# Optimization experiments

Measured on AMD Instinct MI355X. Metric: run time of the kernel, lower is better.

The kernel has to match this reference:

```python
import jax, jax.numpy as jnp
import numpy as np

B, C, H, W = 4, 256, 64, 64
N = H * W


def _c1(Wt, x, b=None):
    # 1x1 conv2d: Wt [out,in], x [B,in,H,W]
    r = jnp.einsum('oi,bihw->bohw', Wt, x)
    return r if b is None else r + b[None, :, None, None]


def setup_inputs() -> dict:
    key = jax.random.key(0)
    ks = jax.random.split(key, 32)
    s = 0.01  # torch init: normal(0, 0.01)
    d = {
        'x': jax.random.normal(ks[0], (B, C, H, W), jnp.float32),
        'y': jax.random.normal(ks[1], (B, C, H, W), jnp.float32),
        'z': jax.random.normal(ks[2], (B, C, 6, 6), jnp.float32),
        'm': jax.random.normal(ks[3], (B, C, 3, 3), jnp.float32),
        'Wv':  jax.random.normal(ks[4], (C, C), jnp.float32) * s,   # conv_value, no bias
        'Wv2': jax.random.normal(ks[5], (C, C), jnp.float32) * s,   # conv_value_2, no bias
        'Wq':  jax.random.normal(ks[6], (C, C), jnp.float32) * s,
        'bq':  jnp.zeros((C,), jnp.float32),
        'Wk':  jax.random.normal(ks[7], (C, C), jnp.float32) * s,
        'bk':  jnp.zeros((C,), jnp.float32),
        'Wq2': jax.random.normal(ks[8], (C, C), jnp.float32) * s,
        'bq2': jnp.zeros((C,), jnp.float32),
        'Wk2': jax.random.normal(ks[9], (C, C), jnp.float32) * s,
        'bk2': jnp.zeros((C,), jnp.float32),
        'Win1': jax.random.normal(ks[10], (C, C), jnp.float32) * s,
        'bin1': jnp.zeros((C,), jnp.float32),
        'Win3': jax.random.normal(ks[11], (C, C), jnp.float32) * s,
        'bin3': jnp.zeros((C,), jnp.float32),
        'Wtr':  jax.random.normal(ks[12], (2 * C, 2 * C), jnp.float32) * s,
        'btr':  jnp.zeros((2 * C,), jnp.float32),
        'Wout2': jax.random.normal(ks[13], (C, C), jnp.float32) * s,
        'bout2': jnp.zeros((C,), jnp.float32),
        'Wout3': jax.random.normal(ks[14], (C, C), jnp.float32) * s,
        'bout3': jnp.zeros((C,), jnp.float32),
        'Wfc': jax.random.normal(ks[15], (36, 9), jnp.float32) * (1.0 / 3.0),  # nn.Linear(9,36)
        'bfc': jnp.zeros((36,), jnp.float32),
        # gammas init to 0 in torch, which zeroes the attention branch; use
        # nonzero values so the baseline exercises the full graph.
        'gamma':  jnp.full((1,), 0.5, jnp.float32),
        'gamma2': jnp.full((1,), 0.5, jnp.float32),
    }
    return d


def reference(x, y, z, m, Wv, Wv2, Wq, bq, Wk, bk, Wq2, bq2, Wk2, bk2,
              Win1, bin1, Win3, bin3, Wtr, btr, Wout2, bout2, Wout3, bout3,
              Wfc, bfc, gamma, gamma2):
    Bs, Cc, Hh, Ww = x.shape
    Nn = Hh * Ww
    # conv_value on y, z, m (no bias)
    yv = _c1(Wv, y)
    zv = _c1(Wv, z)
    mv = _c1(Wv, m)
    y_line = yv.reshape(Bs, Cc, Nn)            # [B,C,N]
    z_line = zv.reshape(Bs, Cc, 36)            # [B,C,36]
    m_line = mv.reshape(Bs, Cc, 9) @ Wfc.T + bfc   # [B,C,36]
    m_line = jnp.transpose(m_line, (0, 2, 1))      # [B,36,C]
    fuse_mz = jnp.einsum('bcn,bnd->bcd', z_line, m_line)      # [B,C,C]
    fuse_mzy = jnp.einsum('bcd,bdn->bcn', fuse_mz, y_line).reshape(yv.shape) + yv  # [B,C,H,W]

    value = fuse_mzy.reshape(Bs, Cc, Nn)                      # [B,C,N]
    value_2 = _c1(Wv2, x).reshape(Bs, Cc, Nn)
    query = _c1(Wq, x, bq).reshape(Bs, Cc, Nn)
    key = _c1(Wk, fuse_mzy, bk).reshape(Bs, Cc, Nn)
    query_2 = _c1(Wq2, x, bq2).reshape(Bs, Cc, Nn)
    key_2 = _c1(Wk2, x, bk2).reshape(Bs, Cc, Nn)

    # branch 1: Q^T K -> softmax over keys -> @ V^T
    sim = jax.nn.softmax(jnp.einsum('bcn,bcm->bnm', query, key), axis=2)
    out_sim = jnp.einsum('bnm,bcm->bcn', sim, value).reshape(Bs, Cc, Hh, Ww)
    out_sim = gamma[0] * out_sim

    # branch 2
    sim2 = jax.nn.softmax(jnp.einsum('bcn,bcm->bnm', query_2, key_2), axis=2)
    out_sim_2 = jnp.einsum('bnm,bcm->bcn', sim2, value_2).reshape(Bs, Cc, Hh, Ww)
    out_sim_2 = gamma2[0] * out_sim_2

    # sigmoid-gated fusion
    H_1 = _c1(Win1, out_sim, bin1)
    H_3 = _c1(Win3, out_sim_2, bin3)
    H_tra = _c1(Wtr, jnp.concatenate([H_1, H_3], axis=1), btr)
    H_5 = jax.nn.sigmoid(_c1(Wout2, H_tra[:, :Cc], bout2))
    H_6 = jax.nn.sigmoid(_c1(Wout3, H_tra[:, Cc:], bout3))
    H_all = jax.nn.softmax(jnp.stack([H_5, H_6], axis=0), axis=0)
    return H_all[0] * out_sim + H_all[1] * out_sim_2 + x
```

## Files before the change

### kernel.cpp

```cpp
#include <hip/hip_runtime.h>

typedef unsigned short u16;
typedef unsigned int   u32;
typedef int   v4i __attribute__((ext_vector_type(4)));
typedef float v4f __attribute__((ext_vector_type(4)));

__device__ __forceinline__ float b2f(u16 v) {
    union { unsigned u; float f; } t; t.u = ((unsigned)v) << 16; return t.f;
}
__device__ __forceinline__ u16 f2b(float f) {
    union { float f; unsigned u; } t; t.f = f;
    unsigned r = (t.u + 0x7FFFu + ((t.u >> 16) & 1u)) >> 16;
    return (u16)r;
}
__device__ __forceinline__ u16 f2b_trunc(float f) {
    union { float f; unsigned u; } t; t.f = f;
    return (u16)(t.u >> 16);
}
__device__ __forceinline__ v4f mfma16(v4i a, v4i b, v4f c) {
    asm("v_mfma_f32_16x16x32_bf16 %0, %1, %2, %0" : "+v"(c) : "v"(a), "v"(b));
    return c;
}
__device__ __forceinline__ void gload16(const u16* g, u16* l) {
    __builtin_amdgcn_global_load_lds(
        (const __attribute__((address_space(1))) unsigned int*)g,
        (__attribute__((address_space(3))) unsigned int*)l,
        16, 0, 0);
}

struct WCvt { const float* s[9]; u16* d[9]; int n[9]; };
__global__ void cvt_weights(WCvt p) {
    int wi = blockIdx.y;
    int i = blockIdx.x * 256 + threadIdx.x;
    if (i < p.n[wi]) p.d[wi][i] = f2b(p.s[wi][i]);
}

__global__ void cvt_t(const float* __restrict__ W1, const float* __restrict__ W3,
                      u16* __restrict__ T1, u16* __restrict__ T3)
{
    const int zz = blockIdx.z;
    const float* src = zz ? W3 : W1;
    u16* dst = zz ? T3 : T1;
    __shared__ float t[32][33];
    const int r0 = blockIdx.x * 32, c0 = blockIdx.y * 32;
    const int tx = threadIdx.x, ty = threadIdx.y;
#pragma unroll
    for (int i = 0; i < 4; i++)
        t[ty + i * 8][tx] = src[(long)(r0 + ty + i * 8) * 256 + c0 + tx];
    __syncthreads();
#pragma unroll
    for (int i = 0; i < 4; i++)
        dst[(long)(c0 + ty + i * 8) * 256 + r0 + tx] = f2b(t[tx][ty + i * 8]);
}

__global__ void bias_btr(const float* __restrict__ Wtr, const float* __restrict__ bin1,
                         const float* __restrict__ bin3, const float* __restrict__ btr,
                         float* __restrict__ btr_eff)
{
    const int j = blockIdx.x, k = threadIdx.x;
    float v = Wtr[(long)j * 512 + k] * bin1[k] + Wtr[(long)j * 512 + 256 + k] * bin3[k];
    v += __shfl_xor(v, 1); v += __shfl_xor(v, 2); v += __shfl_xor(v, 4);
    v += __shfl_xor(v, 8); v += __shfl_xor(v, 16); v += __shfl_xor(v, 32);
    __shared__ float part[4];
    if ((k & 63) == 0) part[k >> 6] = v;
    __syncthreads();
    if (k == 0) btr_eff[j] = btr[j] + part[0] + part[1] + part[2] + part[3];
}

__global__ void bias_r56(const float* __restrict__ Wout2, const float* __restrict__ Wout3,
                         const float* __restrict__ bout2, const float* __restrict__ bout3,
                         const float* __restrict__ btr_eff,
                         float* __restrict__ r5, float* __restrict__ r6)
{
    const int j = blockIdx.x, k = threadIdx.x;
    float v = (j < 256) ? Wout2[(long)j * 256 + k] * btr_eff[k]
                        : Wout3[(long)(j - 256) * 256 + k] * btr_eff[256 + k];
    v += __shfl_xor(v, 1); v += __shfl_xor(v, 2); v += __shfl_xor(v, 4);
    v += __shfl_xor(v, 8); v += __shfl_xor(v, 16); v += __shfl_xor(v, 32);
    __shared__ float part[4];
    if ((k & 63) == 0) part[k >> 6] = v;
    __syncthreads();
    if (k == 0) {
        float s = part[0] + part[1] + part[2] + part[3];
        if (j < 256) r5[j] = bout2[j] + s;
        else         r6[j - 256] = bout3[j - 256] + s;
    }
}

__global__ __launch_bounds__(256) void transpose_cvt(
    const float* __restrict__ x, const float* __restrict__ y,
    u16* __restrict__ xt, u16* __restrict__ yt)
{
    const int z = blockIdx.z, t = z >> 2, b = z & 3;
    const float* src = t ? y : x;
    u16* dst = t ? yt : xt;
    __shared__ float tile[32][33];
    const int nt = blockIdx.x * 32, ct = blockIdx.y * 32;
    const int tx = threadIdx.x, ty = threadIdx.y;
#pragma unroll
    for (int i = 0; i < 4; i++)
        tile[ty + i * 8][tx] = src[((long)b * 256 + ct + ty + i * 8) * 4096 + nt + tx];
    __syncthreads();
#pragma unroll
    for (int i = 0; i < 4; i++)
        dst[((long)b * 4096 + nt + ty + i * 8) * 256 + ct + tx] = f2b(tile[tx][ty + i * 8]);
}

__global__ void small_zm(const float* __restrict__ z, const float* __restrict__ m,
                         const float* __restrict__ Wv, const float* __restrict__ Wfc,
                         const float* __restrict__ bfc,
                         float* __restrict__ zv, float* __restrict__ mline)
{
    const int o = blockIdx.x, b = blockIdx.y, tid = threadIdx.x;
    __shared__ float wrow[256];
    __shared__ float mvs[9];
    for (int i = tid; i < 256; i += 64) wrow[i] = Wv[o * 256 + i];
    __syncthreads();
    if (tid < 36) {
        float s = 0.f;
        for (int c = 0; c < 256; c++) s += wrow[c] * z[((long)b * 256 + c) * 36 + tid];
        zv[((long)b * 256 + o) * 36 + tid] = s;
    }
    if (tid < 9) {
        float s = 0.f;
        for (int c = 0; c < 256; c++) s += wrow[c] * m[((long)b * 256 + c) * 9 + tid];
        mvs[tid] = s;
    }
    __syncthreads();
    if (tid < 36) {
        float s = bfc[tid];
        for (int k = 0; k < 9; k++) s += mvs[k] * Wfc[tid * 9 + k];
        mline[((long)b * 256 + o) * 36 + tid] = s;
    }
}

__global__ void small_F(const float* __restrict__ zv, const float* __restrict__ mline,
                        u16* __restrict__ Fb, u16* __restrict__ FbT)
{
    const int c = blockIdx.x, b = blockIdx.y, d = threadIdx.x;
    const float* zr = zv + ((long)b * 256 + c) * 36;
    const float* mr = mline + ((long)b * 256 + d) * 36;
    float s = (c == d) ? 1.f : 0.f;
    for (int n = 0; n < 36; n++) s += zr[n] * mr[n];
    u16 v = f2b(s);
    Fb[((long)b * 256 + c) * 256 + d] = v;
    FbT[((long)b * 256 + d) * 256 + c] = v;
}

struct GDesc {
    const u16* X; const u16* W; const float* bias;
    u16* outT; u16* outN;
    long xbs, wbs, otbs, onbs;
    int ldx, ldw, ldot, ldon, K, rows;
};
struct GJob { GDesc d[12]; int oblk; };

__global__ __launch_bounds__(256) void gemm_tn(GJob j) {
    const int di = blockIdx.y / j.oblk;
    const int o0 = (blockIdx.y % j.oblk) * 128;
    const GDesc g = j.d[di];
    const int b = blockIdx.z;
    const int n0 = blockIdx.x * 128;
    if (n0 >= g.rows) return;
    const int tid = threadIdx.x, lane = tid & 63, w = tid >> 6;
    const int l15 = lane & 15, lg = lane >> 4;
    const int wr = (w >> 1) * 64, wc = (w & 1) * 64;

    __shared__ __align__(16) u16 As[2][4096];
    __shared__ __align__(16) u16 Bs[2][4096];

    const int sr = w * 32 + (lane >> 2);
    const int sc = (lane & 3) * 8;
    const u16* Xb_ = g.X + b * g.xbs;
    const u16* Wp_ = g.W + b * g.wbs;

    auto STAGE = [&](int buf, int ks) {
#pragma unroll
        for (int i = 0; i < 2; i++) {
            gload16(Xb_ + (long)(n0 + sr + i * 16) * g.ldx + ks * 32 + sc,
                    &As[buf][w * 1024 + i * 512]);
            gload16(Wp_ + (long)(o0 + sr + i * 16) * g.ldw + ks * 32 + sc,
                    &Bs[buf][w * 1024 + i * 512]);
        }
    };

    v4f acc[4][4];
    for (int oi = 0; oi < 4; oi++) {
        float bv = g.bias ? g.bias[o0 + wc + oi * 16 + l15] : 0.f;
        for (int mi = 0; mi < 4; mi++) acc[mi][oi] = (v4f){bv, bv, bv, bv};
    }

    const int steps = g.K >> 5;
    STAGE(0, 0);
    __syncthreads();
    for (int ks = 0; ks < steps; ks++) {
        const int cur = ks & 1;
        if (ks + 1 < steps) STAGE(cur ^ 1, ks + 1);
        v4i a[4], bb[4];
#pragma unroll
        for (int mi = 0; mi < 4; mi++)
            a[mi] = *(const v4i*)&As[cur][(wr + mi * 16 + l15) * 32 + lg * 8];
#pragma unroll
        for (int oi = 0; oi < 4; oi++)
            bb[oi] = *(const v4i*)&Bs[cur][(wc + oi * 16 + l15) * 32 + lg * 8];
#pragma unroll
        for (int mi = 0; mi < 4; mi++)
#pragma unroll
            for (int oi = 0; oi < 4; oi++)
                acc[mi][oi] = mfma16(a[mi], bb[oi], acc[mi][oi]);
        __syncthreads();
    }

    for (int mi = 0; mi < 4; mi++)
        for (int oi = 0; oi < 4; oi++) {
            int nn = n0 + wr + mi * 16 + lg * 4;
            int oo = o0 + wc + oi * 16 + l15;
            if (g.outT) {
                u16* p = g.outT + b * g.otbs + (long)nn * g.ldot + oo;
#pragma unroll
                for (int r = 0; r < 4; r++) p[(long)r * g.ldot] = f2b(acc[mi][oi][r]);
            }
            if (g.outN) {
                ushort4 pk;
                pk.x = f2b(acc[mi][oi][0]); pk.y = f2b(acc[mi][oi][1]);
                pk.z = f2b(acc[mi][oi][2]); pk.w = f2b(acc[mi][oi][3]);
                *(ushort4*)(g.outN + b * g.onbs + (long)oo * g.ldon + nn) = pk;
            }
        }
}

__global__ __launch_bounds__(256) void attn_kernel(
    const u16* __restrict__ qtA, const u16* __restrict__ ktA, const u16* __restrict__ vA,
    u16* __restrict__ otA, u16* __restrict__ onA, const float* __restrict__ gA,
    const u16* __restrict__ qtB, const u16* __restrict__ ktB, const u16* __restrict__ vB,
    u16* __restrict__ otB, u16* __restrict__ onB, const float* __restrict__ gB)
{
    const int wg = blockIdx.x;
    const int qb = wg >> 3, code = wg & 7;
    const int br = code & 1, b = code >> 1;
    const u16* Qt = br ? qtB : qtA;
    const u16* Kt = br ? ktB : ktA;
    const u16* V  = br ? vB  : vA;
    u16* Ot = br ? otB : otA;
    u16* On = br ? onB : onA;
    const float gamma = br ? gB[0] : gA[0];
    const long bs = (long)4096 * 256;
    const u16* Qb = Qt + b * bs;
    const u16* Kb = Kt + b * bs;
    const u16* Vb = V + b * bs;
    u16* Otb = Ot + b * bs;
    u16* Onb = On + b * bs;

    const int tid = threadIdx.x, lane = tid & 63, w = tid >> 6;
    const int l15 = lane & 15, lg = lane >> 4;

    __shared__ __align__(16) u16 Ksh[4][8192];
    __shared__ __align__(16) u16 P[2][64][56];
    __shared__ float den[64];

    v4i qf[8];
    const u16* qp = Qb + (long)(qb * 64 + w * 16 + l15) * 256 + lg * 8;
#pragma unroll
    for (int ks = 0; ks < 8; ks++) qf[ks] = *(const v4i*)(qp + ks * 32);

    v4f oacc[4][4];
    for (int ci = 0; ci < 4; ci++)
        for (int qi = 0; qi < 4; qi++) oacc[ci][qi] = (v4f){0.f, 0.f, 0.f, 0.f};
    float dacc[4] = {0.f, 0.f, 0.f, 0.f};

    const u16* vb = Vb + (long)(w * 64 + l15) * 4096 + lg * 8;
    v4i vfA[4], vfB[4];

    const int srow = w * 8 + (lane >> 5);
    const int scolB = (lane & 31) * 16;

    auto STAGE = [&](int buf, int t) {
        const u16* base = Kb + (long)t * 8192;
        u16* lb = &Ksh[buf][w * 2048];
#pragma unroll
        for (int i = 0; i < 4; i++) {
            int row = srow + i * 2;
            int colB = scolB ^ ((row & 7) << 4);
            gload16(base + row * 256 + (colB >> 1), lb + i * 512);
        }
    };
    auto VLOAD = [&](v4i (&vf)[4], int t) {
#pragma unroll
        for (int ci = 0; ci < 4; ci++)
            vf[ci] = *(const v4i*)(vb + (long)ci * 16 * 4096 + t * 32);
    };

    STAGE(0, 0);
    STAGE(1, 1);
    STAGE(2, 2);
    VLOAD(vfA, 0);
    asm volatile("s_waitcnt vmcnt(12)" ::: "memory");
    __builtin_amdgcn_s_barrier();
    __builtin_amdgcn_sched_barrier(0);

    auto ITER = [&](int mb, v4i (&vcur)[4], v4i (&vnxt)[4]) {
        const u16* kb = &Ksh[mb & 3][0];
        u16* Pc = &P[mb & 1][0][0];

        v4f l0a = {0,0,0,0}, l0b = {0,0,0,0}, l1a = {0,0,0,0}, l1b = {0,0,0,0};
        __builtin_amdgcn_s_setprio(1);
#pragma unroll
        for (int ks = 0; ks < 4; ks++) {
            int c0 = (ks * 64 + lg * 16) ^ ((l15 & 7) << 4);
            v4i k0 = *(const v4i*)(kb + l15 * 256 + (c0 >> 1));
            v4i k1 = *(const v4i*)(kb + (16 + l15) * 256 + (c0 >> 1));
            l0a = mfma16(qf[ks], k0, l0a);
            l1a = mfma16(qf[ks], k1, l1a);
        }
#pragma unroll
        for (int ks = 4; ks < 8; ks++) {
            int c0 = (ks * 64 + lg * 16) ^ ((l15 & 7) << 4);
            v4i k0 = *(const v4i*)(kb + l15 * 256 + (c0 >> 1));
            v4i k1 = *(const v4i*)(kb + (16 + l15) * 256 + (c0 >> 1));
            l0b = mfma16(qf[ks], k0, l0b);
            l1b = mfma16(qf[ks], k1, l1b);
        }
        __builtin_amdgcn_s_setprio(0);
        v4f lacc0 = l0a + l0b, lacc1 = l1a + l1b;

#pragma unroll
        for (int r = 0; r < 4; r++) {
            float e0 = __expf(lacc0[r]);
            float e1 = __expf(lacc1[r]);
            dacc[r] += e0 + e1;
            Pc[(w * 16 + lg * 4 + r) * 56 + l15]      = f2b_trunc(e0);
            Pc[(w * 16 + lg * 4 + r) * 56 + 16 + l15] = f2b_trunc(e1);
        }

        if (mb < 127) VLOAD(vnxt, mb + 1);
        if (mb < 125) STAGE((mb + 3) & 3, mb + 3);

        if (mb <= 124)      asm volatile("s_waitcnt vmcnt(12) lgkmcnt(0)" ::: "memory");
        else if (mb == 125) asm volatile("s_waitcnt vmcnt(8) lgkmcnt(0)" ::: "memory");
        else if (mb == 126) asm volatile("s_waitcnt vmcnt(4) lgkmcnt(0)" ::: "memory");
        else                asm volatile("s_waitcnt vmcnt(0) lgkmcnt(0)" ::: "memory");
        __builtin_amdgcn_s_barrier();
        __builtin_amdgcn_sched_barrier(0);

        v4i pf[4];
#pragma unroll
        for (int qi = 0; qi < 4; qi++)
            pf[qi] = *(const v4i*)(Pc + (qi * 16 + l15) * 56 + lg * 8);
        __builtin_amdgcn_s_setprio(1);
#pragma unroll
        for (int ci = 0; ci < 4; ci++)
#pragma unroll
            for (int qi = 0; qi < 4; qi++)
                oacc[ci][qi] = mfma16(vcur[ci], pf[qi], oacc[ci][qi]);
        __builtin_amdgcn_s_setprio(0);
    };

    for (int mb2 = 0; mb2 < 64; ++mb2) {
        ITER(2 * mb2,     vfA, vfB);
        ITER(2 * mb2 + 1, vfB, vfA);
    }

#pragma unroll
    for (int r = 0; r < 4; r++) {
        float s = dacc[r];
        s += __shfl_xor(s, 1); s += __shfl_xor(s, 2);
        s += __shfl_xor(s, 4); s += __shfl_xor(s, 8);
        if (l15 == 0) den[w * 16 + lg * 4 + r] = s;
    }
    __syncthreads();

    for (int qi = 0; qi < 4; qi++) {
        int q = qi * 16 + l15;
        float sc = gamma / den[q];
        int n = qb * 64 + q;
        for (int ci = 0; ci < 4; ci++) {
            int c0 = w * 64 + ci * 16 + lg * 4;
            ushort4 pk;
            pk.x = f2b(oacc[ci][qi][0] * sc);
            pk.y = f2b(oacc[ci][qi][1] * sc);
            pk.z = f2b(oacc[ci][qi][2] * sc);
            pk.w = f2b(oacc[ci][qi][3] * sc);
            *(ushort4*)(Otb + (long)n * 256 + c0) = pk;
            Onb[(long)(c0 + 0) * 4096 + n] = pk.x;
            Onb[(long)(c0 + 1) * 4096 + n] = pk.y;
            Onb[(long)(c0 + 2) * 4096 + n] = pk.z;
            Onb[(long)(c0 + 3) * 4096 + n] = pk.w;
        }
    }
}

__global__ __launch_bounds__(256) void gate2_gemm(
    const u16* __restrict__ Ot, const u16* __restrict__ O2t,
    const u16* __restrict__ PQ, const float* __restrict__ r5, const float* __restrict__ r6,
    const u16* __restrict__ On, const u16* __restrict__ O2n,
    const float* __restrict__ x, float* __restrict__ out)
{
    const int bz = blockIdx.z;
    const int n0 = blockIdx.x * 64, c0 = blockIdx.y * 64;
    const int tid = threadIdx.x, lane = tid & 63, w = tid >> 6;
    const int l15 = lane & 15, lg = lane >> 4;
    const int wcc = (w >> 1) * 32, wnn = (w & 1) * 32;
    const long NC = 4096L * 256;
    const long arow = c0 + wcc + l15;
    const u16* pa5 = PQ + arow * 256 + lg * 8;
    const u16* qa5 = PQ + 65536 + arow * 256 + lg * 8;
    const u16* pa6 = PQ + 131072 + arow * 256 + lg * 8;
    const u16* qa6 = PQ + 196608 + arow * 256 + lg * 8;
    const u16* bo  = Ot  + bz * NC + (long)(n0 + wnn + l15) * 256 + lg * 8;
    const u16* bo2 = O2t + bz * NC + (long)(n0 + wnn + l15) * 256 + lg * 8;

    v4f a5[2][2], a6[2][2];
    for (int mi = 0; mi < 2; mi++)
        for (int oi = 0; oi < 2; oi++) {
            a5[mi][oi] = (v4f){0, 0, 0, 0};
            a6[mi][oi] = (v4f){0, 0, 0, 0};
        }
#pragma unroll 4
    for (int k = 0; k < 256; k += 32) {
        v4i bb[2], w5[2], w6[2];
#pragma unroll
        for (int oi = 0; oi < 2; oi++) bb[oi] = *(const v4i*)(bo + (long)oi * 16 * 256 + k);
#pragma unroll
        for (int mi = 0; mi < 2; mi++) {
            w5[mi] = *(const v4i*)(pa5 + (long)mi * 16 * 256 + k);
            w6[mi] = *(const v4i*)(pa6 + (long)mi * 16 * 256 + k);
        }
#pragma unroll
        for (int mi = 0; mi < 2; mi++)
#pragma unroll
            for (int oi = 0; oi < 2; oi++) {
                a5[mi][oi] = mfma16(w5[mi], bb[oi], a5[mi][oi]);
                a6[mi][oi] = mfma16(w6[mi], bb[oi], a6[mi][oi]);
            }
    }
#pragma unroll 4
    for (int k = 0; k < 256; k += 32) {
        v4i bb[2], w5[2], w6[2];
#pragma unroll
        for (int oi = 0; oi < 2; oi++) bb[oi] = *(const v4i*)(bo2 + (long)oi * 16 * 256 + k);
#pragma unroll
        for (int mi = 0; mi < 2; mi++) {
            w5[mi] = *(const v4i*)(qa5 + (long)mi * 16 * 256 + k);
            w6[mi] = *(const v4i*)(qa6 + (long)mi * 16 * 256 + k);
        }
#pragma unroll
        for (int mi = 0; mi < 2; mi++)
#pragma unroll
            for (int oi = 0; oi < 2; oi++) {
                a5[mi][oi] = mfma16(w5[mi], bb[oi], a5[mi][oi]);
                a6[mi][oi] = mfma16(w6[mi], bb[oi], a6[mi][oi]);
            }
    }
    for (int mi = 0; mi < 2; mi++) {
        float r5v[4], r6v[4];
#pragma unroll
        for (int r = 0; r < 4; r++) {
            int c = c0 + wcc + mi * 16 + lg * 4 + r;
            r5v[r] = r5[c]; r6v[r] = r6[c];
        }
        for (int oi = 0; oi < 2; oi++) {
            int n = n0 + wnn + oi * 16 + l15;
#pragma unroll
            for (int r = 0; r < 4; r++) {
                int c = c0 + wcc + mi * 16 + lg * 4 + r;
                long base = bz * NC + (long)c * 4096 + n;
                float ov  = b2f(On[base]);
                float ov2 = b2f(O2n[base]);
                float xv  = x[((long)bz * 256 + c) * 4096 + n];
                float s5 = 1.f / (1.f + __expf(-(a5[mi][oi][r] + r5v[r])));
                float s6 = 1.f / (1.f + __expf(-(a6[mi][oi][r] + r6v[r])));
                float w0 = 1.f / (1.f + __expf(s6 - s5));
                out[((long)bz * 256 + c) * 4096 + n] = w0 * ov + (1.f - w0) * ov2 + xv;
            }
        }
    }
}

extern "C" void kernel_launch(void* const* d_in, const int* in_sizes, int n_in,
                              void* d_out, int out_size, void* d_ws, size_t ws_size,
                              hipStream_t stream)
{
    const float* x     = (const float*)d_in[0];
    const float* y     = (const float*)d_in[1];
    const float* z     = (const float*)d_in[2];
    const float* m     = (const float*)d_in[3];
    const float* Wv    = (const float*)d_in[4];
    const float* Wv2   = (const float*)d_in[5];
    const float* Wq    = (const float*)d_in[6];
    const float* bq    = (const float*)d_in[7];
    const float* Wk    = (const float*)d_in[8];
    const float* bk    = (const float*)d_in[9];
    const float* Wq2   = (const float*)d_in[10];
    const float* bq2   = (const float*)d_in[11];
    const float* Wk2   = (const float*)d_in[12];
    const float* bk2   = (const float*)d_in[13];
    const float* Win1  = (const float*)d_in[14];
    const float* bin1  = (const float*)d_in[15];
    const float* Win3  = (const float*)d_in[16];
    const float* bin3  = (const float*)d_in[17];
    const float* Wtr   = (const float*)d_in[18];
    const float* btr   = (const float*)d_in[19];
    const float* Wout2 = (const float*)d_in[20];
    const float* bout2 = (const float*)d_in[21];
    const float* Wout3 = (const float*)d_in[22];
    const float* bout3 = (const float*)d_in[23];
    const float* Wfc   = (const float*)d_in[24];
    const float* bfc   = (const float*)d_in[25];
    const float* gamma  = (const float*)d_in[26];
    const float* gamma2 = (const float*)d_in[27];

    char* ws = (char*)d_ws;
    u16* Wb[6];
    for (int i = 0; i < 6; i++) Wb[i] = (u16*)(ws + (size_t)i * 131072);
    u16* Wout2b = (u16*)(ws + 786432);
    u16* Wout3b = (u16*)(ws + 917504);
    u16* Win1T  = (u16*)(ws + 1048576);
    u16* Win3T  = (u16*)(ws + 1179648);
    u16* Fb   = (u16*)(ws + 1310720);
    u16* FbT  = (u16*)(ws + 1835008);
    u16* Gk   = (u16*)(ws + 2359296);
    u16* PQ   = (u16*)(ws + 2883584);
    u16* Tt   = (u16*)(ws + 3407872);
    float* btr_eff = (float*)(ws + 3932160);
    float* r5 = (float*)(ws + 3934208);
    float* r6 = (float*)(ws + 3935232);
    auto SLOT = [&](int i) { return ws + 4194304 + (size_t)i * 8388608; };
    u16* xt  = (u16*)SLOT(0);
    u16* yt  = (u16*)SLOT(1);
    u16* yvt = (u16*)SLOT(2);
    u16* fmn = (u16*)SLOT(4);
    u16* v2n = (u16*)SLOT(5);
    u16* qt  = (u16*)SLOT(6);
    u16* kt  = (u16*)SLOT(7);
    u16* q2t = (u16*)SLOT(8);
    u16* k2t = (u16*)SLOT(9);
    u16* O2n = (u16*)SLOT(0);
    u16* Ot_ = (u16*)SLOT(1);
    u16* On_ = (u16*)SLOT(2);
    u16* O2t = (u16*)SLOT(3);
    u16* Wtrb   = (u16*)SLOT(3);
    float* zv    = (float*)(SLOT(3) + 524288);
    float* mline = (float*)(SLOT(3) + 671744);

    const long NC = 4096L * 256, CC = 65536;

    {
        WCvt wc;
        const float* wsrc[9] = {Wv, Wv2, Wq, Wk, Wq2, Wk2, Wout2, Wout3, Wtr};
        u16* wdst[9] = {Wb[0], Wb[1], Wb[2], Wb[3], Wb[4], Wb[5], Wout2b, Wout3b, Wtrb};
        for (int i = 0; i < 9; i++) { wc.s[i] = wsrc[i]; wc.d[i] = wdst[i]; wc.n[i] = (i == 8) ? 262144 : 65536; }
        cvt_weights<<<dim3(1024, 9), 256, 0, stream>>>(wc);
    }
    cvt_t<<<dim3(8, 8, 2), dim3(32, 8), 0, stream>>>(Win1, Win3, Win1T, Win3T);

    bias_btr<<<512, 256, 0, stream>>>(Wtr, bin1, bin3, btr, btr_eff);
    bias_r56<<<512, 256, 0, stream>>>(Wout2, Wout3, bout2, bout3, btr_eff, r5, r6);

    transpose_cvt<<<dim3(128, 8, 8), dim3(32, 8), 0, stream>>>(x, y, xt, yt);

    small_zm<<<dim3(256, 4), 64, 0, stream>>>(z, m, Wv, Wfc, bfc, zv, mline);
    small_F<<<dim3(256, 4), 256, 0, stream>>>(zv, mline, Fb, FbT);

    auto mkdesc = [](const u16* X, int ldx, long xbs, const u16* W, int ldw, long wbs,
                     const float* bias, u16* outT, int ldot, long otbs,
                     u16* outN, int ldon, long onbs, int K, int rows) {
        GDesc g; g.X = X; g.W = W; g.bias = bias; g.outT = outT; g.outN = outN;
        g.xbs = xbs; g.wbs = wbs; g.otbs = otbs; g.onbs = onbs;
        g.ldx = ldx; g.ldw = ldw; g.ldot = ldot; g.ldon = ldon; g.K = K; g.rows = rows;
        return g;
    };

    {
        GJob j{}; j.oblk = 2;
        j.d[0] = mkdesc(yt, 256, NC, Wb[0], 256, 0, nullptr, yvt, 256, NC, nullptr, 0, 0, 256, 4096);
        j.d[1] = mkdesc(xt, 256, NC, Wb[2], 256, 0, bq,  qt,  256, NC, nullptr, 0, 0, 256, 4096);
        j.d[2] = mkdesc(xt, 256, NC, Wb[4], 256, 0, bq2, q2t, 256, NC, nullptr, 0, 0, 256, 4096);
        j.d[3] = mkdesc(xt, 256, NC, Wb[5], 256, 0, bk2, k2t, 256, NC, nullptr, 0, 0, 256, 4096);
        j.d[4] = mkdesc(xt, 256, NC, Wb[1], 256, 0, nullptr, nullptr, 0, 0, v2n, 4096, NC, 256, 4096);
        j.d[5] = mkdesc(Wb[3], 256, 0, FbT, 256, CC, nullptr, Gk, 256, CC, nullptr, 0, 0, 256, 256);
        for (int yy = 0; yy < 4; yy++) {
            const u16* Xw = Wtrb + ((yy >> 1) ? 131072 : 0) + ((yy & 1) ? 256 : 0);
            const u16* Ww = (yy & 1) ? Win3T : Win1T;
            j.d[6 + yy] = mkdesc(Xw, 512, 0, Ww, 256, 0, nullptr,
                                 nullptr, 0, 0, Tt + yy * 65536, 256, 0, 256, 256);
        }
        gemm_tn<<<dim3(32, 20, 4), 256, 0, stream>>>(j);
    }
    {
        GJob j{}; j.oblk = 2;
        j.d[0] = mkdesc(yvt, 256, NC, Fb, 256, CC, nullptr, nullptr, 0, 0, fmn, 4096, NC, 256, 4096);
        j.d[1] = mkdesc(yvt, 256, NC, Gk, 256, CC, bk, kt, 256, NC, nullptr, 0, 0, 256, 4096);
        for (int yy = 0; yy < 4; yy++) {
            const u16* Xw = (yy >> 1) ? Wout3b : Wout2b;
            j.d[2 + yy] = mkdesc(Xw, 256, 0, Tt + yy * 65536, 256, 0, nullptr,
                                 PQ + yy * 65536, 256, 0, nullptr, 0, 0, 256, 256);
        }
        gemm_tn<<<dim3(32, 12, 4), 256, 0, stream>>>(j);
    }

    attn_kernel<<<dim3(512), 256, 0, stream>>>(qt, kt, fmn, Ot_, On_, gamma,
                                               q2t, k2t, v2n, O2t, O2n, gamma2);

    gate2_gemm<<<dim3(64, 4, 4), 256, 0, stream>>>(Ot_, O2t, PQ, r5, r6,
                                                   On_, O2n, x, (float*)d_out);
}
```

Baseline: 335.8 us.

## Split attention work across 8 waves instead of 4 per workgroup

Doubles the attention workgroup to 512 threads. Each pair of waves now shares a 16-query slice and splits the 32-key tile in halves for the QK^T step, and each wave owns 32 output channels instead of 64 for the PV step. The softmax denominator becomes two partial sums combined at the end. The goal is more waves for latency hiding and fewer registers per wave (oacc drops from 16 to 8 vectors). In exchange, Q fragments are loaded redundantly by paired waves and a larger group must meet at each barrier.

```diff
diff --git a/kernel.cpp b/kernel.cpp
--- a/kernel.cpp
+++ b/kernel.cpp
@@ -229,7 +229,7 @@
         }
 }
 
-__global__ __launch_bounds__(256) void attn_kernel(
+__global__ __launch_bounds__(512, 4) void attn_kernel(
     const u16* __restrict__ qtA, const u16* __restrict__ ktA, const u16* __restrict__ vA,
     u16* __restrict__ otA, u16* __restrict__ onA, const float* __restrict__ gA,
     const u16* __restrict__ qtB, const u16* __restrict__ ktB, const u16* __restrict__ vB,
@@ -253,40 +253,41 @@
 
     const int tid = threadIdx.x, lane = tid & 63, w = tid >> 6;
     const int l15 = lane & 15, lg = lane >> 4;
+    const int qh = w >> 1, kh = w & 1;
 
     __shared__ __align__(16) u16 Ksh[4][8192];
-    __shared__ __align__(16) u16 P[2][64][56];
-    __shared__ float den[64];
+    __shared__ __align__(16) u16 P[2][64][40];
+    __shared__ float denp[2][64];
 
     v4i qf[8];
-    const u16* qp = Qb + (long)(qb * 64 + w * 16 + l15) * 256 + lg * 8;
+    const u16* qp = Qb + (long)(qb * 64 + qh * 16 + l15) * 256 + lg * 8;
 #pragma unroll
     for (int ks = 0; ks < 8; ks++) qf[ks] = *(const v4i*)(qp + ks * 32);
 
-    v4f oacc[4][4];
-    for (int ci = 0; ci < 4; ci++)
+    v4f oacc[2][4];
+    for (int ci = 0; ci < 2; ci++)
         for (int qi = 0; qi < 4; qi++) oacc[ci][qi] = (v4f){0.f, 0.f, 0.f, 0.f};
     float dacc[4] = {0.f, 0.f, 0.f, 0.f};
 
-    const u16* vb = Vb + (long)(w * 64 + l15) * 4096 + lg * 8;
-    v4i vfA[4], vfB[4];
-
-    const int srow = w * 8 + (lane >> 5);
+    const u16* vb = Vb + (long)(w * 32 + l15) * 4096 + lg * 8;
+    v4i vfA[2], vfB[2];
+
+    const int srow = w * 4 + (lane >> 5);
     const int scolB = (lane & 31) * 16;
 
     auto STAGE = [&](int buf, int t) {
         const u16* base = Kb + (long)t * 8192;
-        u16* lb = &Ksh[buf][w * 2048];
-#pragma unroll
-        for (int i = 0; i < 4; i++) {
+        u16* lb = &Ksh[buf][w * 1024];
+#pragma unroll
+        for (int i = 0; i < 2; i++) {
             int row = srow + i * 2;
             int colB = scolB ^ ((row & 7) << 4);
             gload16(base + row * 256 + (colB >> 1), lb + i * 512);
         }
     };
-    auto VLOAD = [&](v4i (&vf)[4], int t) {
-#pragma unroll
-        for (int ci = 0; ci < 4; ci++)
+    auto VLOAD = [&](v4i (&vf)[2], int t) {
+#pragma unroll
+        for (int ci = 0; ci < 2; ci++)
             vf[ci] = *(const v4i*)(vb + (long)ci * 16 * 4096 + t * 32);
     };
 
@@ -294,50 +295,44 @@
     STAGE(1, 1);
     STAGE(2, 2);
     VLOAD(vfA, 0);
-    asm volatile("s_waitcnt vmcnt(12)" ::: "memory");
+    asm volatile("s_waitcnt vmcnt(6)" ::: "memory");
     __builtin_amdgcn_s_barrier();
     __builtin_amdgcn_sched_barrier(0);
 
-    auto ITER = [&](int mb, v4i (&vcur)[4], v4i (&vnxt)[4]) {
+    auto ITER = [&](int mb, v4i (&vcur)[2], v4i (&vnxt)[2]) {
         const u16* kb = &Ksh[mb & 3][0];
         u16* Pc = &P[mb & 1][0][0];
 
-        v4f l0a = {0,0,0,0}, l0b = {0,0,0,0}, l1a = {0,0,0,0}, l1b = {0,0,0,0};
+        v4f la = {0,0,0,0}, lb2 = {0,0,0,0};
         __builtin_amdgcn_s_setprio(1);
 #pragma unroll
         for (int ks = 0; ks < 4; ks++) {
             int c0 = (ks * 64 + lg * 16) ^ ((l15 & 7) << 4);
-            v4i k0 = *(const v4i*)(kb + l15 * 256 + (c0 >> 1));
-            v4i k1 = *(const v4i*)(kb + (16 + l15) * 256 + (c0 >> 1));
-            l0a = mfma16(qf[ks], k0, l0a);
-            l1a = mfma16(qf[ks], k1, l1a);
+            v4i kf = *(const v4i*)(kb + (kh * 16 + l15) * 256 + (c0 >> 1));
+            la = mfma16(qf[ks], kf, la);
         }
 #pragma unroll
         for (int ks = 4; ks < 8; ks++) {
             int c0 = (ks * 64 + lg * 16) ^ ((l15 & 7) << 4);
-            v4i k0 = *(const v4i*)(kb + l15 * 256 + (c0 >> 1));
-            v4i k1 = *(const v4i*)(kb + (16 + l15) * 256 + (c0 >> 1));
-            l0b = mfma16(qf[ks], k0, l0b);
-            l1b = mfma16(qf[ks], k1, l1b);
+            v4i kf = *(const v4i*)(kb + (kh * 16 + l15) * 256 + (c0 >> 1));
+            lb2 = mfma16(qf[ks], kf, lb2);
         }
         __builtin_amdgcn_s_setprio(0);
-        v4f lacc0 = l0a + l0b, lacc1 = l1a + l1b;
+        v4f lacc = la + lb2;
 
 #pragma unroll
         for (int r = 0; r < 4; r++) {
-            float e0 = __expf(lacc0[r]);
-            float e1 = __expf(lacc1[r]);
-            dacc[r] += e0 + e1;
-            Pc[(w * 16 + lg * 4 + r) * 56 + l15]      = f2b_trunc(e0);
-            Pc[(w * 16 + lg * 4 + r) * 56 + 16 + l15] = f2b_trunc(e1);
+            float e = __expf(lacc[r]);
+            dacc[r] += e;
+            Pc[(qh * 16 + lg * 4 + r) * 40 + kh * 16 + l15] = f2b_trunc(e);
         }
 
         if (mb < 127) VLOAD(vnxt, mb + 1);
         if (mb < 125) STAGE((mb + 3) & 3, mb + 3);
 
-        if (mb <= 124)      asm volatile("s_waitcnt vmcnt(12) lgkmcnt(0)" ::: "memory");
-        else if (mb == 125) asm volatile("s_waitcnt vmcnt(8) lgkmcnt(0)" ::: "memory");
-        else if (mb == 126) asm volatile("s_waitcnt vmcnt(4) lgkmcnt(0)" ::: "memory");
+        if (mb <= 124)      asm volatile("s_waitcnt vmcnt(6) lgkmcnt(0)" ::: "memory");
+        else if (mb == 125) asm volatile("s_waitcnt vmcnt(4) lgkmcnt(0)" ::: "memory");
+        else if (mb == 126) asm volatile("s_waitcnt vmcnt(2) lgkmcnt(0)" ::: "memory");
         else                asm volatile("s_waitcnt vmcnt(0) lgkmcnt(0)" ::: "memory");
         __builtin_amdgcn_s_barrier();
         __builtin_amdgcn_sched_barrier(0);
@@ -345,10 +340,10 @@
         v4i pf[4];
 #pragma unroll
         for (int qi = 0; qi < 4; qi++)
-            pf[qi] = *(const v4i*)(Pc + (qi * 16 + l15) * 56 + lg * 8);
+            pf[qi] = *(const v4i*)(Pc + (qi * 16 + l15) * 40 + lg * 8);
         __builtin_amdgcn_s_setprio(1);
 #pragma unroll
-        for (int ci = 0; ci < 4; ci++)
+        for (int ci = 0; ci < 2; ci++)
 #pragma unroll
             for (int qi = 0; qi < 4; qi++)
                 oacc[ci][qi] = mfma16(vcur[ci], pf[qi], oacc[ci][qi]);
@@ -365,16 +360,16 @@
         float s = dacc[r];
         s += __shfl_xor(s, 1); s += __shfl_xor(s, 2);
         s += __shfl_xor(s, 4); s += __shfl_xor(s, 8);
-        if (l15 == 0) den[w * 16 + lg * 4 + r] = s;
+        if (l15 == 0) denp[kh][qh * 16 + lg * 4 + r] = s;
     }
     __syncthreads();
 
     for (int qi = 0; qi < 4; qi++) {
         int q = qi * 16 + l15;
-        float sc = gamma / den[q];
+        float sc = gamma / (denp[0][q] + denp[1][q]);
         int n = qb * 64 + q;
-        for (int ci = 0; ci < 4; ci++) {
-            int c0 = w * 64 + ci * 16 + lg * 4;
+        for (int ci = 0; ci < 2; ci++) {
+            int c0 = w * 32 + ci * 16 + lg * 4;
             ushort4 pk;
             pk.x = f2b(oacc[ci][qi][0] * sc);
             pk.y = f2b(oacc[ci][qi][1] * sc);
@@ -598,7 +593,7 @@
         gemm_tn<<<dim3(32, 12, 4), 256, 0, stream>>>(j);
     }
 
-    attn_kernel<<<dim3(512), 256, 0, stream>>>(qt, kt, fmn, Ot_, On_, gamma,
+    attn_kernel<<<dim3(512), 512, 0, stream>>>(qt, kt, fmn, Ot_, On_, gamma,
                                                q2t, k2t, v2n, O2t, O2n, gamma2);
 
     gate2_gemm<<<dim3(64, 4, 4), 256, 0, stream>>>(Ot_, O2t, PQ, r5, r6,
```

After: 404.1 us. 1.2x slower.
